# Performance work log

Hardware: AMD Instinct MI355X
Metric: run time of the kernel (lower is better)

## Reference

```python
import jax, jax.numpy as jnp
import numpy as np

WIDTH = 16
HID = 512
NHEADS = 8
DK = HID // NHEADS
NLAYERS = 2
NHIGHWAY = 2
B = 4
S = 1024
PAD = S + 2 * WIDTH  # padded sequence length


def setup_inputs() -> dict:
    key = jax.random.key(0)
    ks = jax.random.split(key, 10)
    sc = 0.02
    f32 = jnp.float32
    return {
        "inputs": jax.random.normal(ks[0], (B, S, HID), f32),
        "masks": jnp.ones((B, S), jnp.int32),
        # 4 linears (q,k,v,out) per attention, torch Linear layout [out,in]
        "fw_lin_w": sc * jax.random.normal(ks[1], (NLAYERS, 4, HID, HID), f32),
        "fw_lin_b": jnp.zeros((NLAYERS, 4, HID), f32),
        "bw_lin_w": sc * jax.random.normal(ks[2], (NLAYERS, 4, HID, HID), f32),
        "bw_lin_b": jnp.zeros((NLAYERS, 4, HID), f32),
        # Highway: Linear(H, 2H); [:H]=nonlinear part, [H:]=gate (gate bias init 1)
        "fw_hw_w": sc * jax.random.normal(ks[3], (NLAYERS, NHIGHWAY, 2 * HID, HID), f32),
        "fw_hw_b": jnp.zeros((NLAYERS, NHIGHWAY, 2 * HID), f32).at[:, :, HID:].set(1.0),
        "bw_hw_w": sc * jax.random.normal(ks[4], (NLAYERS, NHIGHWAY, 2 * HID, HID), f32),
        "bw_hw_b": jnp.zeros((NLAYERS, NHIGHWAY, 2 * HID), f32).at[:, :, HID:].set(1.0),
        # learned boundary paddings, [width, hidden] per layer
        "fw_pad": sc * jax.random.normal(ks[5], (NLAYERS, WIDTH, HID), f32),
        "bw_pad": sc * jax.random.normal(ks[6], (NLAYERS, WIDTH, HID), f32),
        # relative-position weight vectors, [width+1] per layer
        "fw_rel": sc * jax.random.normal(ks[7], (NLAYERS, WIDTH + 1), f32),
        "bw_rel": sc * jax.random.normal(ks[8], (NLAYERS, WIDTH + 1), f32),
    }


def _band_masks():
    i = jnp.arange(PAD)[:, None]
    j = jnp.arange(PAD)[None, :]
    mf = (j <= i) & (j >= i - WIDTH - 1)          # causal band, width+2 wide
    mb = (j >= i) & (j <= i + WIDTH + 1)          # flipped (anticausal) band
    return mf, mb


def _mha(x, w, b, mask):
    # x: [B, PAD, HID]; w: [4, HID, HID]; b: [4, HID]
    def heads(t):
        return t.reshape(B, PAD, NHEADS, DK).transpose(0, 2, 1, 3)  # bhpd
    q = heads(x @ w[0].T + b[0])
    k = heads(x @ w[1].T + b[1])
    v = heads(x @ w[2].T + b[2])
    scores = jnp.einsum('bhqd,bhkd->bhqk', q, k) / np.sqrt(DK).astype(np.float32)
    scores = jnp.where(mask[None, None], scores, jnp.float32(-1e9))
    p = jax.nn.softmax(scores, axis=-1)
    o = jnp.einsum('bhqk,bhkd->bhqd', p, v)
    o = o.transpose(0, 2, 1, 3).reshape(B, PAD, HID)
    return o @ w[3].T + b[3]


def _highway(x, w, b):
    for i in range(NHIGHWAY):
        proj = x @ w[i].T + b[i]
        nonlin = jax.nn.relu(proj[..., :HID])
        gate = jax.nn.sigmoid(proj[..., HID:])
        x = gate * x + (1.0 - gate) * nonlin
    return x


def _rel(x, w, offset):
    # sum_k w[k] * x[:, offset+k : offset+k+S, :]  (width+1=17 fixed taps)
    out = w[0] * jax.lax.dynamic_slice_in_dim(x, offset, S, 1)
    for k in range(1, WIDTH + 1):
        out = out + w[k] * jax.lax.dynamic_slice_in_dim(x, offset + k, S, 1)
    return out


def _forward(inputs, fw_lin_w, fw_lin_b, bw_lin_w, bw_lin_b,
             fw_hw_w, fw_hw_b, bw_hw_w, bw_hw_b,
             fw_pad, bw_pad, fw_rel, bw_rel):
    mf, mb = _band_masks()
    f = inputs
    bk = inputs
    outs = []
    for l in range(NLAYERS):
        fp = jnp.broadcast_to(fw_pad[l][None], (B, WIDTH, HID))
        bp = jnp.broadcast_to(bw_pad[l][None], (B, WIDTH, HID))
        f_padded = jnp.concatenate([fp, f, bp], axis=1)    # [B, PAD, HID]
        b_padded = jnp.concatenate([fp, bk, bp], axis=1)
        fa = _mha(f_padded, fw_lin_w[l], fw_lin_b[l], mf)
        ba = _mha(b_padded, bw_lin_w[l], bw_lin_b[l], mb)
        # per-step: out[t] = attn[t+width] + rel-position windowed combination
        fo = fa[:, WIDTH:WIDTH + S, :] + _rel(fa, fw_rel[l], 0)
        bo = ba[:, WIDTH:WIDTH + S, :] + _rel(ba, bw_rel[l], WIDTH)
        f = _highway(fo, fw_hw_w[l], fw_hw_b[l])
        bk = _highway(bo, bw_hw_w[l], bw_hw_b[l])
        outs.append(jnp.concatenate([f, bk], axis=-1))
    return jnp.stack(outs, axis=0)  # [NLAYERS, B, S, 2*HID]


def reference(inputs, masks, fw_lin_w, fw_lin_b, bw_lin_w, bw_lin_b,
              fw_hw_w, fw_hw_b, bw_hw_w, bw_hw_b,
              fw_pad, bw_pad, fw_rel, bw_rel):
    # masks is accepted (as in the torch signature) but unused in the body
    return _forward(inputs, fw_lin_w, fw_lin_b, bw_lin_w, bw_lin_b,
                    fw_hw_w, fw_hw_b, bw_hw_w, bw_hw_b,
                    fw_pad, bw_pad, fw_rel, bw_rel)
```

## Files before the change

### kernel.cpp

```cpp
#include <hip/hip_runtime.h>

using s8 = __attribute__((ext_vector_type(8))) short;
using f4 = __attribute__((ext_vector_type(4))) float;

constexpr int WIDTH   = 16;
constexpr int HID     = 512;
constexpr int NHEADS  = 8;
constexpr int DK      = 64;
constexpr int NLAYERS = 2;
constexpr int NHW     = 2;
constexpr int B       = 4;
constexpr int S       = 1024;
constexpr int PAD     = S + 2 * WIDTH;
constexpr int RS      = 1024;
constexpr int K2      = 1024;

__device__ inline unsigned short f2bf(float x) {
    union { float f; unsigned u; } c; c.f = x;
    unsigned r = c.u + 0x7fffu + ((c.u >> 16) & 1u);
    return (unsigned short)(r >> 16);
}
__device__ inline float bf2f(unsigned short h) {
    union { float f; unsigned u; } c; c.u = ((unsigned)h) << 16; return c.f;
}
__device__ inline void split2(float x, unsigned short& h, unsigned short& l) {
    h = f2bf(x);
    l = f2bf(x - bf2f(h));
}
__device__ inline void store_split4(unsigned short* dst, float4 v) {
    unsigned short h[4], l[4];
    split2(v.x, h[0], l[0]); split2(v.y, h[1], l[1]);
    split2(v.z, h[2], l[2]); split2(v.w, h[3], l[3]);
    uint2 hp, lp;
    hp.x = h[0] | ((unsigned)h[1] << 16); hp.y = h[2] | ((unsigned)h[3] << 16);
    lp.x = l[0] | ((unsigned)l[1] << 16); lp.y = l[2] | ((unsigned)l[3] << 16);
    *(uint2*)(dst)       = hp;
    *(uint2*)(dst + 512) = lp;
}

__global__ __launch_bounds__(256) void build_pad_split(
    const float* __restrict__ src0, const float* __restrict__ src1,
    const float* __restrict__ front, const float* __restrict__ back,
    unsigned short* __restrict__ d0, unsigned short* __restrict__ d1)
{
    const float* x = blockIdx.z ? src1 : src0;
    unsigned short* xp2 = blockIdx.z ? d1 : d0;
    int idx = blockIdx.x * 256 + threadIdx.x;
    int c4 = idx & 127;
    int rest = idx >> 7;
    int p = rest % PAD;
    int b = rest / PAD;
    float4 val;
    if (p < WIDTH) {
        val = *(const float4*)(front + (size_t)p * HID + c4 * 4);
    } else if (p < WIDTH + S) {
        val = *(const float4*)(x + ((size_t)b * S + (p - WIDTH)) * HID + c4 * 4);
    } else {
        val = *(const float4*)(back + (size_t)(p - WIDTH - S) * HID + c4 * 4);
    }
    store_split4(xp2 + (size_t)(b * PAD + p) * RS + c4 * 4, val);
}

__global__ __launch_bounds__(256) void conv_w(
    const float* __restrict__ s0, const float* __restrict__ s1,
    unsigned short* __restrict__ w0, unsigned short* __restrict__ w1)
{
    const float* src = blockIdx.z ? s1 : s0;
    unsigned short* dst = blockIdx.z ? w1 : w0;
    int idx = blockIdx.x * 256 + threadIdx.x;
    int c4 = idx & 127;
    int r  = idx >> 7;
    float4 v = *(const float4*)(src + (size_t)r * HID + c4 * 4);
    store_split4(dst + (size_t)r * RS + c4 * 4, v);
}

__global__ __launch_bounds__(256) void conv_all(
    const float* __restrict__ fw_lin_w, const float* __restrict__ bw_lin_w,
    const float* __restrict__ fw_hw_w,  const float* __restrict__ bw_hw_w,
    unsigned short* __restrict__ w2all)
{
    int idx = blockIdx.x * 256 + threadIdx.x;
    int c4 = idx & 127;
    int r  = idx >> 7;
    int l  = r >> 12;
    int rr = r & 4095;
    const float* lin = blockIdx.z ? bw_lin_w : fw_lin_w;
    const float* hw  = blockIdx.z ? bw_hw_w  : fw_hw_w;
    const float* src = (rr < 2048)
        ? lin + ((size_t)l * 2048 + rr) * HID
        : hw  + ((size_t)l * 2048 + (rr - 2048)) * HID;
    float4 v = *(const float4*)(src + c4 * 4);
    store_split4(w2all + ((size_t)blockIdx.z * 8192 + r) * RS + c4 * 4, v);
}

__global__ __launch_bounds__(256) void gemm_split(
    const unsigned short* __restrict__ A0, const unsigned short* __restrict__ B0,
    const float* __restrict__ bias0, float* __restrict__ C0,
    const unsigned short* __restrict__ A1, const unsigned short* __restrict__ B1,
    const float* __restrict__ bias1, float* __restrict__ C1,
    int N)
{
    const unsigned short* A  = blockIdx.z ? A1 : A0;
    const unsigned short* Bw = blockIdx.z ? B1 : B0;
    const float* bias        = blockIdx.z ? bias1 : bias0;
    float* C                 = blockIdx.z ? C1 : C0;

    __shared__ unsigned short Als[128 * 32];
    __shared__ unsigned short Bls[128 * 32];

    const int tid  = threadIdx.x;
    const int wave = tid >> 6;
    const int lane = tid & 63;
    const int bm = blockIdx.y * 128;
    const int bn = blockIdx.x * 128;
    const int wm = (wave >> 1) * 64;
    const int wn = (wave & 1) * 64;

    const int c0 = wave * 2, c1 = wave * 2 + 1;
    const int lr = lane >> 2;
    const int kg = ((lane & 3) + (lr >> 1)) & 3;
    const int sr0 = c0 * 16 + lr;
    const int sr1 = c1 * 16 + lr;
    const int sc  = kg * 8;
    const unsigned short* Ag0 = A  + (size_t)(bm + sr0) * RS + sc;
    const unsigned short* Ag1 = A  + (size_t)(bm + sr1) * RS + sc;
    const unsigned short* Bg0 = Bw + (size_t)(bn + sr0) * RS + sc;
    const unsigned short* Bg1 = Bw + (size_t)(bn + sr1) * RS + sc;
    const int ls0 = c0 * 512;
    const int ls1 = c1 * 512;

    const int fr = lane & 15;
    const int q  = lane >> 4;
    const int rslot = (4 * fr + ((q - (fr >> 1)) & 3)) * 8;

    f4 acc[4][4] = {};

    for (int k0 = 0; k0 < K2; k0 += 32) {
        const int aoff = k0;
        const int boff = (k0 < 512) ? k0 : (k0 - 512);
        __builtin_amdgcn_global_load_lds(
            (const __attribute__((address_space(1))) void*)(Ag0 + aoff),
            (__attribute__((address_space(3))) void*)&Als[ls0], 16, 0, 0);
        __builtin_amdgcn_global_load_lds(
            (const __attribute__((address_space(1))) void*)(Ag1 + aoff),
            (__attribute__((address_space(3))) void*)&Als[ls1], 16, 0, 0);
        __builtin_amdgcn_global_load_lds(
            (const __attribute__((address_space(1))) void*)(Bg0 + boff),
            (__attribute__((address_space(3))) void*)&Bls[ls0], 16, 0, 0);
        __builtin_amdgcn_global_load_lds(
            (const __attribute__((address_space(1))) void*)(Bg1 + boff),
            (__attribute__((address_space(3))) void*)&Bls[ls1], 16, 0, 0);
        __syncthreads();

        s8 a[4], b[4];
        #pragma unroll
        for (int i = 0; i < 4; ++i)
            a[i] = *(const s8*)&Als[((wm >> 4) + i) * 512 + rslot];
        #pragma unroll
        for (int j = 0; j < 4; ++j)
            b[j] = *(const s8*)&Bls[((wn >> 4) + j) * 512 + rslot];
        #pragma unroll
        for (int i = 0; i < 4; ++i)
            #pragma unroll
            for (int j = 0; j < 4; ++j)
                acc[i][j] = __builtin_amdgcn_mfma_f32_16x16x32_bf16(
                    a[i], b[j], acc[i][j], 0, 0, 0);
        __syncthreads();
    }

    const int col = lane & 15;
    const int rb  = (lane >> 4) * 4;
    #pragma unroll
    for (int j = 0; j < 4; ++j) {
        float bj = bias[bn + wn + j * 16 + col];
        #pragma unroll
        for (int i = 0; i < 4; ++i) {
            size_t base = (size_t)(bm + wm + i * 16 + rb) * N + (bn + wn + j * 16 + col);
            #pragma unroll
            for (int r = 0; r < 4; ++r)
                C[base + (size_t)r * N] = acc[i][j][r] + bj;
        }
    }
}

__global__ __launch_bounds__(256) void banded_attn(
    const float* __restrict__ Q0, const float* __restrict__ Q1,
    unsigned short* __restrict__ O0, unsigned short* __restrict__ O1,
    int dir0)
{
    const float* QKV = blockIdx.z ? Q1 : Q0;
    unsigned short* O2 = blockIdx.z ? O1 : O0;
    int backward = dir0 + blockIdx.z;

    int w    = blockIdx.x * 4 + (threadIdx.x >> 6);
    int lane = threadIdx.x & 63;
    int i  = w % PAD;
    int bh = w / PAD;
    int h  = bh & (NHEADS - 1);
    int b  = bh / NHEADS;

    int jlo, n;
    if (backward) { jlo = i; n = min(WIDTH + 2, PAD - i); }
    else          { jlo = max(0, i - WIDTH - 1); n = i - jlo + 1; }

    const int s = lane >> 4;
    const int d = lane & 15;
    const size_t rowbase = (size_t)(b * PAD) * 1536;
    const int colq = h * DK;

    float4 q4 = *(const float4*)(QKV + rowbase + (size_t)i * 1536 + colq + 4 * d);

    float sc[5];
    #pragma unroll
    for (int m = 0; m < 5; ++m) {
        int t  = 4 * m + s;
        int tc = t < n ? t : n - 1;
        float4 kv = *(const float4*)(QKV + rowbase + (size_t)(jlo + tc) * 1536
                                     + 512 + colq + 4 * d);
        float p = q4.x * kv.x + q4.y * kv.y + q4.z * kv.z + q4.w * kv.w;
        p += __shfl_xor(p, 1);
        p += __shfl_xor(p, 2);
        p += __shfl_xor(p, 4);
        p += __shfl_xor(p, 8);
        sc[m] = p * 0.125f;
    }

    float sv[WIDTH + 2];
    #pragma unroll
    for (int t = 0; t < WIDTH + 2; ++t) {
        float v = __shfl(sc[t >> 2], (t & 3) << 4);
        sv[t] = (t < n) ? v : -1e30f;
    }
    float mx = sv[0];
    #pragma unroll
    for (int t = 1; t < WIDTH + 2; ++t) mx = fmaxf(mx, sv[t]);
    float denom = 0.f;
    #pragma unroll
    for (int t = 0; t < WIDTH + 2; ++t) { sv[t] = __expf(sv[t] - mx); denom += sv[t]; }
    float inv = 1.0f / denom;

    float od0 = 0.f, od1 = 0.f;
    #pragma unroll
    for (int t = 0; t < WIDTH + 2; t += 2) {
        int tc0 = t     < n ? t     : n - 1;
        int tc1 = t + 1 < n ? t + 1 : n - 1;
        od0 += sv[t]     * QKV[rowbase + (size_t)(jlo + tc0) * 1536 + 1024 + colq + lane];
        od1 += sv[t + 1] * QKV[rowbase + (size_t)(jlo + tc1) * 1536 + 1024 + colq + lane];
    }
    float od = (od0 + od1) * inv;

    unsigned short hh, ll;
    split2(od, hh, ll);
    size_t ro = (size_t)(b * PAD + i) * RS + colq + lane;
    O2[ro] = hh; O2[ro + 512] = ll;
}

__global__ __launch_bounds__(256) void rel_combine(
    const float* __restrict__ a0, const float* __restrict__ a1,
    const float* __restrict__ w0, const float* __restrict__ w1,
    unsigned short* __restrict__ f0, unsigned short* __restrict__ f1,
    int off0, int off1)
{
    const float* att = blockIdx.z ? a1 : a0;
    const float* w   = blockIdx.z ? w1 : w0;
    unsigned short* fo2 = blockIdx.z ? f1 : f0;
    int offset = blockIdx.z ? off1 : off0;

    int idx = blockIdx.x * 256 + threadIdx.x;
    int c4 = idx & 127;
    int rest = idx >> 7;
    int t = rest & (S - 1);
    int b = rest >> 10;

    const float* rowbase = att + (size_t)b * PAD * HID + c4 * 4;
    float4 acc = *(const float4*)(rowbase + (size_t)(WIDTH + t) * HID);
    #pragma unroll
    for (int k = 0; k <= WIDTH; ++k) {
        float wk = w[k];
        float4 xv = *(const float4*)(rowbase + (size_t)(offset + k + t) * HID);
        acc.x += wk * xv.x; acc.y += wk * xv.y;
        acc.z += wk * xv.z; acc.w += wk * xv.w;
    }
    store_split4(fo2 + ((size_t)b * S + t) * RS + c4 * 4, acc);
}

__global__ __launch_bounds__(256) void highway_gate(
    const unsigned short* __restrict__ x0, const unsigned short* __restrict__ x1,
    const float* __restrict__ p0, const float* __restrict__ p1,
    float* __restrict__ of0, float* __restrict__ of1,
    unsigned short* __restrict__ o20, unsigned short* __restrict__ o21,
    float* __restrict__ os0, float* __restrict__ os1)
{
    const unsigned short* x2 = blockIdx.z ? x1 : x0;
    const float* proj        = blockIdx.z ? p1 : p0;
    float* outf              = blockIdx.z ? of1 : of0;
    unsigned short* out2     = blockIdx.z ? o21 : o20;
    float* oslice            = blockIdx.z ? os1 : os0;

    int idx = blockIdx.x * 256 + threadIdx.x;
    int c4 = idx & 127;
    int r  = idx >> 7;
    const unsigned short* xr = x2 + (size_t)r * RS + c4 * 4;
    uint2 hp = *(const uint2*)(xr);
    uint2 lp = *(const uint2*)(xr + 512);
    float4 xv;
    xv.x = bf2f((unsigned short)(hp.x & 0xffff)) + bf2f((unsigned short)(lp.x & 0xffff));
    xv.y = bf2f((unsigned short)(hp.x >> 16))    + bf2f((unsigned short)(lp.x >> 16));
    xv.z = bf2f((unsigned short)(hp.y & 0xffff)) + bf2f((unsigned short)(lp.y & 0xffff));
    xv.w = bf2f((unsigned short)(hp.y >> 16))    + bf2f((unsigned short)(lp.y >> 16));

    float4 nl = *(const float4*)(proj + (size_t)r * (2 * HID) + c4 * 4);
    float4 g  = *(const float4*)(proj + (size_t)r * (2 * HID) + HID + c4 * 4);
    float4 o;
    float sg;
    sg = 1.f / (1.f + __expf(-g.x)); o.x = sg * xv.x + (1.f - sg) * fmaxf(nl.x, 0.f);
    sg = 1.f / (1.f + __expf(-g.y)); o.y = sg * xv.y + (1.f - sg) * fmaxf(nl.y, 0.f);
    sg = 1.f / (1.f + __expf(-g.z)); o.z = sg * xv.z + (1.f - sg) * fmaxf(nl.z, 0.f);
    sg = 1.f / (1.f + __expf(-g.w)); o.w = sg * xv.w + (1.f - sg) * fmaxf(nl.w, 0.f);
    if (outf)   *(float4*)(outf + (size_t)idx * 4) = o;
    if (out2)   store_split4(out2 + (size_t)r * RS + c4 * 4, o);
    if (oslice) *(float4*)(oslice + (size_t)r * (2 * HID) + c4 * 4) = o;
}

extern "C" void kernel_launch(void* const* d_in, const int* in_sizes, int n_in,
                              void* d_out, int out_size, void* d_ws, size_t ws_size,
                              hipStream_t stream)
{
    const float* inputs   = (const float*)d_in[0];
    const float* fw_lin_w = (const float*)d_in[2];
    const float* fw_lin_b = (const float*)d_in[3];
    const float* bw_lin_w = (const float*)d_in[4];
    const float* bw_lin_b = (const float*)d_in[5];
    const float* fw_hw_w  = (const float*)d_in[6];
    const float* fw_hw_b  = (const float*)d_in[7];
    const float* bw_hw_w  = (const float*)d_in[8];
    const float* bw_hw_b  = (const float*)d_in[9];
    const float* fw_pad   = (const float*)d_in[10];
    const float* bw_pad   = (const float*)d_in[11];
    const float* fw_rel   = (const float*)d_in[12];
    const float* bw_rel   = (const float*)d_in[13];
    float* out = (float*)d_out;
    float* ws  = (float*)d_ws;

    const size_t BSH  = (size_t)B * S * HID;
    const size_t QKVF = (size_t)B * PAD * 1536;
    const int MP = B * PAD;
    const int MS = B * S;

    const size_t GROUPED_FLOATS = 2 * QKVF + (2 * (size_t)MP * RS + 2 * (size_t)1536 * RS) / 2;
    const size_t WALL_FLOATS    = 2 * QKVF + (2 * (size_t)MP * RS + (size_t)2 * 8192 * RS) / 2;
    const bool wall    = ws_size >= WALL_FLOATS * 4;
    const bool grouped = wall || ws_size >= GROUPED_FLOATS * 4;
    const int G = grouped ? 2 : 1;

    float* f  = ws;
    float* bk = f + BSH;

    float* QKV[2]; float* ATT[2]; float* HWP[2];
    unsigned short* ACT2[2]; unsigned short* W2[2];
    unsigned short* w2all = nullptr;
    if (grouped) {
        QKV[0] = ws;             QKV[1] = ws + QKVF;
        float* extra = ws + 2 * BSH;
        ATT[0] = extra;          ATT[1] = extra + (size_t)MP * HID;
        HWP[0] = extra;          HWP[1] = extra + (size_t)MS * 1024;
        unsigned short* a2 = (unsigned short*)(ws + 2 * QKVF);
        ACT2[0] = a2;            ACT2[1] = a2 + (size_t)MP * RS;
        unsigned short* w2 = a2 + 2 * (size_t)MP * RS;
        if (wall) { w2all = w2; W2[0] = W2[1] = nullptr; }
        else      { W2[0] = w2; W2[1] = w2 + (size_t)1536 * RS; }
    } else {
        float* qkvS = bk + BSH;
        QKV[0] = QKV[1] = qkvS;
        ATT[0] = ATT[1] = qkvS;
        HWP[0] = HWP[1] = qkvS;
        unsigned short* a2 = (unsigned short*)(qkvS + QKVF);
        ACT2[0] = ACT2[1] = a2;
        W2[0] = W2[1] = a2 + (size_t)MP * RS;
    }

    if (wall) {
        conv_all<<<dim3(8192 * 128 / 256, 1, 2), 256, 0, stream>>>(
            fw_lin_w, bw_lin_w, fw_hw_w, bw_hw_w, w2all);
    }
    auto WB = [&](int dir, int l, int seg) -> unsigned short* {
        return w2all + ((size_t)dir * 8192 + (size_t)l * 4096 + seg) * RS;
    };

    for (int l = 0; l < NLAYERS; ++l) {
        const float* LINW[2] = {fw_lin_w + (size_t)l * 4 * HID * HID,
                                bw_lin_w + (size_t)l * 4 * HID * HID};
        const float* LINB[2] = {fw_lin_b + (size_t)l * 4 * HID,
                                bw_lin_b + (size_t)l * 4 * HID};
        const float* HWW[2]  = {fw_hw_w + (size_t)l * NHW * 2 * HID * HID,
                                bw_hw_w + (size_t)l * NHW * 2 * HID * HID};
        const float* HWB[2]  = {fw_hw_b + (size_t)l * NHW * 2 * HID,
                                bw_hw_b + (size_t)l * NHW * 2 * HID};
        const float* RELW[2] = {fw_rel + (size_t)l * (WIDTH + 1),
                                bw_rel + (size_t)l * (WIDTH + 1)};
        const float* front = fw_pad + (size_t)l * WIDTH * HID;
        const float* back  = bw_pad + (size_t)l * WIDTH * HID;
        float* DST[2] = {f, bk};
        float* OSL[2] = {out + (size_t)l * B * S * 2 * HID,
                         out + (size_t)l * B * S * 2 * HID + HID};
        const float* SRC[2] = {(l == 0) ? inputs : f, (l == 0) ? inputs : bk};

        for (int d0 = 0; d0 < 2; d0 += G) {
            const int dB = (G == 2) ? 1 : d0;

            build_pad_split<<<dim3(MP * 128 / 256, 1, G), 256, 0, stream>>>(
                SRC[d0], SRC[dB], front, back, ACT2[0], ACT2[1]);

            unsigned short *wq0, *wq1;
            if (wall) { wq0 = WB(d0, l, 0); wq1 = WB(dB, l, 0); }
            else {
                conv_w<<<dim3(1536 * 128 / 256, 1, G), 256, 0, stream>>>(
                    LINW[d0], LINW[dB], W2[0], W2[1]);
                wq0 = W2[0]; wq1 = W2[1];
            }
            gemm_split<<<dim3(1536 / 128, MP / 128, G), 256, 0, stream>>>(
                ACT2[0], wq0, LINB[d0], QKV[0],
                ACT2[1], wq1, LINB[dB], QKV[1], 1536);

            banded_attn<<<dim3(B * NHEADS * PAD / 4, 1, G), 256, 0, stream>>>(
                QKV[0], QKV[1], ACT2[0], ACT2[1], d0);

            unsigned short *wo0, *wo1;
            if (wall) { wo0 = WB(d0, l, 1536); wo1 = WB(dB, l, 1536); }
            else {
                conv_w<<<dim3(512 * 128 / 256, 1, G), 256, 0, stream>>>(
                    LINW[d0] + 3 * (size_t)HID * HID, LINW[dB] + 3 * (size_t)HID * HID,
                    W2[0], W2[1]);
                wo0 = W2[0]; wo1 = W2[1];
            }
            gemm_split<<<dim3(512 / 128, MP / 128, G), 256, 0, stream>>>(
                ACT2[0], wo0, LINB[d0] + 3 * HID, ATT[0],
                ACT2[1], wo1, LINB[dB] + 3 * HID, ATT[1], 512);

            rel_combine<<<dim3(MS * 128 / 256, 1, G), 256, 0, stream>>>(
                ATT[0], ATT[1], RELW[d0], RELW[dB], ACT2[0], ACT2[1],
                d0 * WIDTH, dB * WIDTH);

            for (int i = 0; i < NHW; ++i) {
                unsigned short *wh0, *wh1;
                if (wall) { wh0 = WB(d0, l, 2048 + 1024 * i); wh1 = WB(dB, l, 2048 + 1024 * i); }
                else {
                    conv_w<<<dim3(1024 * 128 / 256, 1, G), 256, 0, stream>>>(
                        HWW[d0] + (size_t)i * 2 * HID * HID,
                        HWW[dB] + (size_t)i * 2 * HID * HID, W2[0], W2[1]);
                    wh0 = W2[0]; wh1 = W2[1];
                }
                gemm_split<<<dim3(1024 / 128, MS / 128, G), 256, 0, stream>>>(
                    ACT2[0], wh0, HWB[d0] + (size_t)i * 2 * HID, HWP[0],
                    ACT2[1], wh1, HWB[dB] + (size_t)i * 2 * HID, HWP[1], 1024);
                const bool last = (i == NHW - 1);
                highway_gate<<<dim3(MS * 128 / 256, 1, G), 256, 0, stream>>>(
                    ACT2[0], ACT2[1], HWP[0], HWP[1],
                    last ? DST[d0] : (float*)nullptr,
                    last ? DST[dB] : (float*)nullptr,
                    last ? (unsigned short*)nullptr : ACT2[0],
                    last ? (unsigned short*)nullptr : ACT2[1],
                    last ? OSL[d0] : (float*)nullptr,
                    last ? OSL[dB] : (float*)nullptr);
            }
        }
    }
}
```

Before: 581.7 us.

## Fuse highway gate into GEMM epilogue with interleaved nonlinear/gate weight rows

Highway weight rows are permuted at conversion time so each 16-column chunk of nonlinear outputs sits next to the matching gate chunk. A new GEMM kernel then computes the sigmoid gate, ReLU and carry blend in its epilogue, which removes the fp32 HWP intermediate round-trip and the separate highway_gate launches. The first highway step writes split-bf16 activations to a new buffer and the second writes the final outputs directly. The epilogue re-reads the A input scattered from global memory, and the path only runs when the full weight buffer fits in the workspace.

```diff
diff --git a/kernel.cpp b/kernel.cpp
--- a/kernel.cpp
+++ b/kernel.cpp
@@ -86,11 +86,23 @@
     int rr = r & 4095;
     const float* lin = blockIdx.z ? bw_lin_w : fw_lin_w;
     const float* hw  = blockIdx.z ? bw_hw_w  : fw_hw_w;
-    const float* src = (rr < 2048)
-        ? lin + ((size_t)l * 2048 + rr) * HID
-        : hw  + ((size_t)l * 2048 + (rr - 2048)) * HID;
+    const float* src;
+    size_t drow;
+    if (rr < 2048) {
+        src  = lin + ((size_t)l * 2048 + rr) * HID;
+        drow = (size_t)blockIdx.z * 8192 + (size_t)l * 4096 + rr;
+    } else {
+        int sub  = rr - 2048;
+        int i_hw = sub >> 10;
+        int rr2  = sub & 1023;
+        int c    = rr2 & 511;
+        int is_g = rr2 >> 9;
+        int p    = ((c >> 4) << 5) + (c & 15) + (is_g << 4);
+        src  = hw + ((size_t)l * 2048 + sub) * HID;
+        drow = (size_t)blockIdx.z * 8192 + (size_t)l * 4096 + 2048 + (i_hw << 10) + p;
+    }
     float4 v = *(const float4*)(src + c4 * 4);
-    store_split4(w2all + ((size_t)blockIdx.z * 8192 + r) * RS + c4 * 4, v);
+    store_split4(w2all + drow * RS + c4 * 4, v);
 }
 
 __global__ __launch_bounds__(256) void gemm_split(
@@ -179,6 +191,116 @@
             #pragma unroll
             for (int r = 0; r < 4; ++r)
                 C[base + (size_t)r * N] = acc[i][j][r] + bj;
+        }
+    }
+}
+
+__global__ __launch_bounds__(256) void gemm_hw_fused(
+    const unsigned short* __restrict__ A0, const unsigned short* __restrict__ B0,
+    const float* __restrict__ hwb0, unsigned short* __restrict__ o2_0,
+    float* __restrict__ dst0, float* __restrict__ osl0,
+    const unsigned short* __restrict__ A1, const unsigned short* __restrict__ B1,
+    const float* __restrict__ hwb1, unsigned short* __restrict__ o2_1,
+    float* __restrict__ dst1, float* __restrict__ osl1,
+    int first)
+{
+    const unsigned short* A  = blockIdx.z ? A1 : A0;
+    const unsigned short* Bw = blockIdx.z ? B1 : B0;
+    const float* hwb         = blockIdx.z ? hwb1 : hwb0;
+    unsigned short* o2       = blockIdx.z ? o2_1 : o2_0;
+    float* dstf              = blockIdx.z ? dst1 : dst0;
+    float* osl               = blockIdx.z ? osl1 : osl0;
+
+    __shared__ unsigned short Als[128 * 32];
+    __shared__ unsigned short Bls[128 * 32];
+
+    const int tid  = threadIdx.x;
+    const int wave = tid >> 6;
+    const int lane = tid & 63;
+    const int bm = blockIdx.y * 128;
+    const int bn = blockIdx.x * 128;
+    const int wm = (wave >> 1) * 64;
+    const int wn = (wave & 1) * 64;
+
+    const int c0 = wave * 2, c1 = wave * 2 + 1;
+    const int lr = lane >> 2;
+    const int kg = ((lane & 3) + (lr >> 1)) & 3;
+    const int sr0 = c0 * 16 + lr;
+    const int sr1 = c1 * 16 + lr;
+    const int sc  = kg * 8;
+    const unsigned short* Ag0 = A  + (size_t)(bm + sr0) * RS + sc;
+    const unsigned short* Ag1 = A  + (size_t)(bm + sr1) * RS + sc;
+    const unsigned short* Bg0 = Bw + (size_t)(bn + sr0) * RS + sc;
+    const unsigned short* Bg1 = Bw + (size_t)(bn + sr1) * RS + sc;
+    const int ls0 = c0 * 512;
+    const int ls1 = c1 * 512;
+
+    const int fr = lane & 15;
+    const int q  = lane >> 4;
+    const int rslot = (4 * fr + ((q - (fr >> 1)) & 3)) * 8;
+
+    f4 acc[4][4] = {};
+
+    for (int k0 = 0; k0 < K2; k0 += 32) {
+        const int aoff = k0;
+        const int boff = (k0 < 512) ? k0 : (k0 - 512);
+        __builtin_amdgcn_global_load_lds(
+            (const __attribute__((address_space(1))) void*)(Ag0 + aoff),
+            (__attribute__((address_space(3))) void*)&Als[ls0], 16, 0, 0);
+        __builtin_amdgcn_global_load_lds(
+            (const __attribute__((address_space(1))) void*)(Ag1 + aoff),
+            (__attribute__((address_space(3))) void*)&Als[ls1], 16, 0, 0);
+        __builtin_amdgcn_global_load_lds(
+            (const __attribute__((address_space(1))) void*)(Bg0 + boff),
+            (__attribute__((address_space(3))) void*)&Bls[ls0], 16, 0, 0);
+        __builtin_amdgcn_global_load_lds(
+            (const __attribute__((address_space(1))) void*)(Bg1 + boff),
+            (__attribute__((address_space(3))) void*)&Bls[ls1], 16, 0, 0);
+        __syncthreads();
+
+        s8 a[4], b[4];
+        #pragma unroll
+        for (int i = 0; i < 4; ++i)
+            a[i] = *(const s8*)&Als[((wm >> 4) + i) * 512 + rslot];
+        #pragma unroll
+        for (int j = 0; j < 4; ++j)
+            b[j] = *(const s8*)&Bls[((wn >> 4) + j) * 512 + rslot];
+        #pragma unroll
+        for (int i = 0; i < 4; ++i)
+            #pragma unroll
+            for (int j = 0; j < 4; ++j)
+                acc[i][j] = __builtin_amdgcn_mfma_f32_16x16x32_bf16(
+                    a[i], b[j], acc[i][j], 0, 0, 0);
+        __syncthreads();
+    }
+
+    const int col = lane & 15;
+    const int rb  = (lane >> 4) * 4;
+    #pragma unroll
+    for (int jp = 0; jp < 2; ++jp) {
+        const int cc = ((bn + wn) >> 1) + jp * 16 + col;
+        const float bnl = hwb[cc];
+        const float bg  = hwb[512 + cc];
+        #pragma unroll
+        for (int i = 0; i < 4; ++i) {
+            #pragma unroll
+            for (int r = 0; r < 4; ++r) {
+                const int row = bm + wm + i * 16 + rb + r;
+                float nl = acc[i][2 * jp][r] + bnl;
+                float g  = acc[i][2 * jp + 1][r] + bg;
+                float xv = bf2f(A[(size_t)row * RS + cc])
+                         + bf2f(A[(size_t)row * RS + cc + 512]);
+                float sg = 1.f / (1.f + __expf(-g));
+                float o  = sg * xv + (1.f - sg) * fmaxf(nl, 0.f);
+                if (first) {
+                    unsigned short hh, ll; split2(o, hh, ll);
+                    o2[(size_t)row * RS + cc]       = hh;
+                    o2[(size_t)row * RS + cc + 512] = ll;
+                } else {
+                    dstf[(size_t)row * HID + cc]      = o;
+                    osl[(size_t)row * (2 * HID) + cc] = o;
+                }
+            }
         }
     }
 }
@@ -358,12 +480,15 @@
 
     float* QKV[2]; float* ATT[2]; float* HWP[2];
     unsigned short* ACT2[2]; unsigned short* W2[2];
+    unsigned short* ACT2B[2] = {nullptr, nullptr};
     unsigned short* w2all = nullptr;
     if (grouped) {
         QKV[0] = ws;             QKV[1] = ws + QKVF;
         float* extra = ws + 2 * BSH;
         ATT[0] = extra;          ATT[1] = extra + (size_t)MP * HID;
         HWP[0] = extra;          HWP[1] = extra + (size_t)MS * 1024;
+        ACT2B[0] = (unsigned short*)extra;
+        ACT2B[1] = ACT2B[0] + (size_t)MS * RS;
         unsigned short* a2 = (unsigned short*)(ws + 2 * QKVF);
         ACT2[0] = a2;            ACT2[1] = a2 + (size_t)MP * RS;
         unsigned short* w2 = a2 + 2 * (size_t)MP * RS;
@@ -441,27 +566,31 @@
                 ATT[0], ATT[1], RELW[d0], RELW[dB], ACT2[0], ACT2[1],
                 d0 * WIDTH, dB * WIDTH);
 
-            for (int i = 0; i < NHW; ++i) {
-                unsigned short *wh0, *wh1;
-                if (wall) { wh0 = WB(d0, l, 2048 + 1024 * i); wh1 = WB(dB, l, 2048 + 1024 * i); }
-                else {
+            if (wall) {
+                gemm_hw_fused<<<dim3(1024 / 128, MS / 128, G), 256, 0, stream>>>(
+                    ACT2[0], WB(d0, l, 2048), HWB[d0], ACT2B[0], nullptr, nullptr,
+                    ACT2[1], WB(dB, l, 2048), HWB[dB], ACT2B[1], nullptr, nullptr, 1);
+                gemm_hw_fused<<<dim3(1024 / 128, MS / 128, G), 256, 0, stream>>>(
+                    ACT2B[0], WB(d0, l, 3072), HWB[d0] + 1024, nullptr, DST[d0], OSL[d0],
+                    ACT2B[1], WB(dB, l, 3072), HWB[dB] + 1024, nullptr, DST[dB], OSL[dB], 0);
+            } else {
+                for (int i = 0; i < NHW; ++i) {
                     conv_w<<<dim3(1024 * 128 / 256, 1, G), 256, 0, stream>>>(
                         HWW[d0] + (size_t)i * 2 * HID * HID,
                         HWW[dB] + (size_t)i * 2 * HID * HID, W2[0], W2[1]);
-                    wh0 = W2[0]; wh1 = W2[1];
+                    gemm_split<<<dim3(1024 / 128, MS / 128, G), 256, 0, stream>>>(
+                        ACT2[0], W2[0], HWB[d0] + (size_t)i * 2 * HID, HWP[0],
+                        ACT2[1], W2[1], HWB[dB] + (size_t)i * 2 * HID, HWP[1], 1024);
+                    const bool last = (i == NHW - 1);
+                    highway_gate<<<dim3(MS * 128 / 256, 1, G), 256, 0, stream>>>(
+                        ACT2[0], ACT2[1], HWP[0], HWP[1],
+                        last ? DST[d0] : (float*)nullptr,
+                        last ? DST[dB] : (float*)nullptr,
+                        last ? (unsigned short*)nullptr : ACT2[0],
+                        last ? (unsigned short*)nullptr : ACT2[1],
+                        last ? OSL[d0] : (float*)nullptr,
+                        last ? OSL[dB] : (float*)nullptr);
                 }
-                gemm_split<<<dim3(1024 / 128, MS / 128, G), 256, 0, stream>>>(
-                    ACT2[0], wh0, HWB[d0] + (size_t)i * 2 * HID, HWP[0],
-                    ACT2[1], wh1, HWB[dB] + (size_t)i * 2 * HID, HWP[1], 1024);
-                const bool last = (i == NHW - 1);
-                highway_gate<<<dim3(MS * 128 / 256, 1, G), 256, 0, stream>>>(
-                    ACT2[0], ACT2[1], HWP[0], HWP[1],
-                    last ? DST[d0] : (float*)nullptr,
-                    last ? DST[dB] : (float*)nullptr,
-                    last ? (unsigned short*)nullptr : ACT2[0],
-                    last ? (unsigned short*)nullptr : ACT2[1],
-                    last ? OSL[d0] : (float*)nullptr,
-                    last ? OSL[dB] : (float*)nullptr);
             }
         }
     }
```

Measured after the change: 564.3 us. 3.0% less time.
